# Kernel tuning notes

Hardware: AMD Instinct MI355X
Metric: run time of the kernel (lower is better)

The kernel has to match this reference:

```python
import jax, jax.numpy as jnp
import numpy as np

B, S, INP, HID = 64, 2048, 512, 512

def setup_inputs() -> dict:
    key = jax.random.key(0)
    ks = jax.random.split(key, 8)
    inp = jax.random.normal(ks[0], (B, INP), dtype=jnp.float32)
    context = jax.random.normal(ks[1], (B, S, INP), dtype=jnp.float32)
    mask = jax.random.randint(ks[2], (B, S), 0, 2) == 1  # True = masked out
    lim_l = 1.0 / np.sqrt(INP)
    Wl = jax.random.uniform(ks[3], (HID, INP), minval=-lim_l, maxval=lim_l, dtype=jnp.float32)
    bl = jax.random.uniform(ks[4], (HID,), minval=-lim_l, maxval=lim_l, dtype=jnp.float32)
    Wc = jax.random.uniform(ks[5], (HID, INP), minval=-lim_l, maxval=lim_l, dtype=jnp.float32)  # Conv1d k=1 weight squeezed
    bc = jax.random.uniform(ks[6], (HID,), minval=-lim_l, maxval=lim_l, dtype=jnp.float32)
    V = jax.random.uniform(ks[7], (HID,), minval=-1.0, maxval=1.0, dtype=jnp.float32)
    return {"inp": inp, "context": context, "mask": mask,
            "Wl": Wl, "bl": bl, "Wc": Wc, "bc": bc, "V": V}

def reference(inp, context, mask, Wl, bl, Wc, bc, V):
    # hid: [B, HID], broadcast over S
    hid = inp @ Wl.T + bl
    # 1x1 Conv1d over permuted context == per-position linear: [B, HID, S]
    ctx = jnp.einsum('bsi,hi->bhs', context, Wc) + bc[None, :, None]
    # additive attention scores: [B, S]
    att = jnp.einsum('h,bhs->bs', V, jnp.tanh(hid[:, :, None] + ctx))
    att = jnp.where(mask, -jnp.inf, att)
    alpha = jax.nn.softmax(att, axis=1)
    # context vector: [B, HID]
    hidden_state = jnp.einsum('bhs,bs->bh', ctx, alpha)
    return (hidden_state, alpha)
```

## Files before the change

kernel.cpp:

```cpp
#include <hip/hip_runtime.h>
#include <hip/hip_bf16.h>
#include <cstdint>
#include <cstddef>

#define B_   64
#define S_   2048
#define INP_ 512
#define HID_ 512

typedef float          floatx4  __attribute__((ext_vector_type(4)));
typedef __bf16         bf16x8   __attribute__((ext_vector_type(8)));
typedef unsigned short ushortx8 __attribute__((ext_vector_type(8)));

__device__ __forceinline__ unsigned short f2bf(float f) {
  unsigned u = __float_as_uint(f);
  u += 0x7FFFu + ((u >> 16) & 1u);
  return (unsigned short)(u >> 16);
}
__device__ __forceinline__ float fast_tanh(float x) {
  float u = __builtin_amdgcn_exp2f(x * 2.88539008177792681472f);
  return 1.0f - 2.0f * __builtin_amdgcn_rcpf(u + 1.0f);
}

__device__ __forceinline__ void gload_lds16(const float* g, float* l) {
  __builtin_amdgcn_global_load_lds(
      (const __attribute__((address_space(1))) unsigned int*)(const void*)g,
      (__attribute__((address_space(3))) unsigned int*)(void*)l, 16, 0, 0);
}

template<int NPART>
__global__ __launch_bounds__(256) void rowdot_kernel(
    const float* __restrict__ W, const float* __restrict__ bias,
    const float* __restrict__ vecs, float* __restrict__ out, int nch)
{
  __shared__ float vs[512];
  const int b = blockIdx.y, t = threadIdx.x;
  const int w = t >> 6, lane = t & 63;
  for (int i = t; i < 512; i += 256) {
    float s;
    if (NPART) {
      s = 0.0f;
      for (int c = 0; c < nch; ++c)
        s += vecs[((size_t)c * B_ + b) * INP_ + i];
    } else {
      s = vecs[(size_t)b * 512 + i];
    }
    vs[i] = s;
  }
  __syncthreads();
  float vl[8];
  #pragma unroll
  for (int j = 0; j < 8; ++j) vl[j] = vs[lane * 8 + j];
  const int h0 = blockIdx.x * 64 + w * 16;
  #pragma unroll
  for (int i = 0; i < 16; ++i) {
    const int h = h0 + i;
    const float4* wr = (const float4*)(W + (size_t)h * 512 + lane * 8);
    float4 w0 = wr[0], w1 = wr[1];
    float d = w0.x*vl[0] + w0.y*vl[1] + w0.z*vl[2] + w0.w*vl[3]
            + w1.x*vl[4] + w1.y*vl[5] + w1.z*vl[6] + w1.w*vl[7];
    #pragma unroll
    for (int off = 32; off; off >>= 1) d += __shfl_xor(d, off);
    if (lane == 0) out[(size_t)b * 512 + h] = bias[h] + d;
  }
}

__global__ void pack_wc_kernel(const float* __restrict__ Wc, unsigned short* __restrict__ pk)
{
  int g = blockIdx.x * 256 + threadIdx.x;
  int l = g & 63, ks = (g >> 6) & 15, m16 = g >> 10;
  int row = m16 * 16 + (l & 15);
  int kb  = ks * 32 + (l >> 4) * 8;
  const float4* s = (const float4*)(Wc + (size_t)row * 512 + kb);
  float4 a = s[0], c = s[1];
  ushortx8 o = { f2bf(a.x), f2bf(a.y), f2bf(a.z), f2bf(a.w),
                 f2bf(c.x), f2bf(c.y), f2bf(c.z), f2bf(c.w) };
  *(ushortx8*)(pk + (size_t)g * 8) = o;
}

__global__ __launch_bounds__(256, 2) void att_gemm_kernel(
    const float* __restrict__ context, const unsigned short* __restrict__ Wc_pk,
    const float* __restrict__ hid, const float* __restrict__ bc,
    const float* __restrict__ V, float* __restrict__ att)
{
  __shared__ alignas(16) float bsf[64 * 128];
  __shared__ float hid_sm[512];
  __shared__ float V_sm[512];
  __shared__ float bc_sm[512];
  __shared__ float att_sm[64];

  const int b    = blockIdx.y;
  const int s0   = blockIdx.x * 64;
  const int t    = threadIdx.x;
  const int lane = t & 63;
  const int w    = t >> 6;
  const int quad = lane >> 4;
  const int l15  = lane & 15;

  for (int i = t; i < 512; i += 256) {
    hid_sm[i] = hid[b * 512 + i];
    V_sm[i]   = V[i];
    bc_sm[i]  = bc[i];
  }
  if (t < 64) att_sm[t] = 0.0f;

  floatx4 acc[8][4];
  #pragma unroll
  for (int m = 0; m < 8; ++m)
    #pragma unroll
    for (int n = 0; n < 4; ++n) { floatx4 z = {0.f,0.f,0.f,0.f}; acc[m][n] = z; }

  const unsigned short* apBase = Wc_pk + (size_t)(w * 8) * 8192 + lane * 8;
  const float* src = context + ((size_t)b * S_ + s0) * INP_;

  for (int phase = 0; phase < 4; ++phase) {
    __syncthreads();
    #pragma unroll
    for (int i = 0; i < 8; ++i) {
      const int row = (w * 8 + i) * 2 + (lane >> 5);
      const int c   = (lane & 31) ^ (row & 7);
      gload_lds16(src + (size_t)row * INP_ + phase * 128 + c * 4,
                  &bsf[(w * 8 + i) * 256]);
    }
    __syncthreads();
    #pragma unroll
    for (int ksl = 0; ksl < 4; ++ksl) {
      const int ksg = phase * 4 + ksl;
      bf16x8 bfr[4];
      #pragma unroll
      for (int n = 0; n < 4; ++n) {
        const int row = n * 16 + l15;
        const int cb  = ksl * 8 + quad * 2;
        const int p0  = cb ^ (row & 7);
        const int p1  = (cb + 1) ^ (row & 7);
        floatx4 f0 = *(const floatx4*)(&bsf[row * 128 + p0 * 4]);
        floatx4 f1 = *(const floatx4*)(&bsf[row * 128 + p1 * 4]);
        bf16x8 r;
        r[0] = (__bf16)f0[0]; r[1] = (__bf16)f0[1];
        r[2] = (__bf16)f0[2]; r[3] = (__bf16)f0[3];
        r[4] = (__bf16)f1[0]; r[5] = (__bf16)f1[1];
        r[6] = (__bf16)f1[2]; r[7] = (__bf16)f1[3];
        bfr[n] = r;
      }
      #pragma unroll
      for (int m = 0; m < 8; ++m) {
        bf16x8 af = *(const bf16x8*)(apBase + (size_t)m * 8192 + (size_t)ksg * 512);
        #pragma unroll
        for (int n = 0; n < 4; ++n)
          acc[m][n] = __builtin_amdgcn_mfma_f32_16x16x32_bf16(af, bfr[n], acc[m][n], 0, 0, 0);
      }
    }
  }

  float attacc[4] = {0.f, 0.f, 0.f, 0.f};
  #pragma unroll
  for (int m = 0; m < 8; ++m) {
    const int hb = w * 128 + m * 16 + quad * 4;
    #pragma unroll
    for (int r = 0; r < 4; ++r) {
      const int h = hb + r;
      const float base = hid_sm[h] + bc_sm[h];
      const float vv = V_sm[h];
      #pragma unroll
      for (int n = 0; n < 4; ++n)
        attacc[n] += vv * fast_tanh(base + acc[m][n][r]);
    }
  }
  #pragma unroll
  for (int n = 0; n < 4; ++n) {
    float v = attacc[n];
    v += __shfl_xor(v, 16);
    v += __shfl_xor(v, 32);
    if (lane < 16) atomicAdd(&att_sm[n * 16 + l15], v);
  }
  __syncthreads();
  if (t < 64) att[b * S_ + s0 + t] = att_sm[t];
}

__global__ void softmax_kernel(const void* __restrict__ mask,
                               const float* __restrict__ att,
                               float* __restrict__ alpha)
{
  __shared__ int flags;
  __shared__ float red[8];
  const int b = blockIdx.x, t = threadIdx.x;
  const int lane = t & 63, w = t >> 6;
  if (t == 0) flags = 0;
  __syncthreads();
  int f = 0;
  const unsigned* mw = (const unsigned*)mask;
  for (int i = t; i < 512; i += 256) {
    unsigned v = mw[i];
    if (v > 1u) f |= 1;
    if (v != 0u && v != 0x3f800000u) f |= 2;
  }
  if (f) atomicOr(&flags, f);
  __syncthreads();
  const int fl = flags;
  const int mode = ((fl & 1) == 0) ? 0 : (((fl & 2) == 0) ? 1 : 2);

  float v[8]; bool msk[8];
  float vmax = -1e30f;
  #pragma unroll
  for (int i = 0; i < 8; ++i) {
    int idx = i * 256 + t;
    bool m;
    if (mode == 0)      m = ((const int*)mask)[b * S_ + idx] != 0;
    else if (mode == 1) m = ((const float*)mask)[b * S_ + idx] != 0.0f;
    else                m = ((const unsigned char*)mask)[b * S_ + idx] != 0;
    msk[i] = m;
    v[i] = att[b * S_ + idx];
    if (!m) vmax = fmaxf(vmax, v[i]);
  }
  #pragma unroll
  for (int off = 32; off; off >>= 1) vmax = fmaxf(vmax, __shfl_xor(vmax, off));
  if (lane == 0) red[w] = vmax;
  __syncthreads();
  vmax = fmaxf(fmaxf(red[0], red[1]), fmaxf(red[2], red[3]));

  float e[8], s = 0.0f;
  #pragma unroll
  for (int i = 0; i < 8; ++i) {
    e[i] = msk[i] ? 0.0f : __builtin_amdgcn_exp2f((v[i] - vmax) * 1.4426950408889634f);
    s += e[i];
  }
  #pragma unroll
  for (int off = 32; off; off >>= 1) s += __shfl_xor(s, off);
  if (lane == 0) red[4 + w] = s;
  __syncthreads();
  s = red[4] + red[5] + red[6] + red[7];
  float rinv = 1.0f / s;
  #pragma unroll
  for (int i = 0; i < 8; ++i)
    alpha[b * S_ + i * 256 + t] = e[i] * rinv;
}

__global__ __launch_bounds__(256) void cbar_kernel(
    const float* __restrict__ context, const float* __restrict__ alpha,
    float* __restrict__ partial, int rows)
{
  __shared__ float a_sm[2048];
  const int b = blockIdx.y, c = blockIdx.x, t = threadIdx.x;
  const int s0 = c * rows;
  for (int i = t; i < rows; i += 256) a_sm[i] = alpha[(size_t)b * S_ + s0 + i];
  __syncthreads();
  const float* base = context + ((size_t)b * S_ + s0) * INP_ + t * 2;
  float ax = 0.f, ay = 0.f;
  #pragma unroll 8
  for (int s = 0; s < rows; ++s) {
    float2 v = *(const float2*)(base + (size_t)s * INP_);
    float a = a_sm[s];
    ax = fmaf(a, v.x, ax);
    ay = fmaf(a, v.y, ay);
  }
  float2 o; o.x = ax; o.y = ay;
  *(float2*)(partial + ((size_t)c * B_ + b) * INP_ + t * 2) = o;
}

extern "C" void kernel_launch(void* const* d_in, const int* in_sizes, int n_in,
                              void* d_out, int out_size, void* d_ws, size_t ws_size,
                              hipStream_t stream)
{
  const float* inp     = (const float*)d_in[0];
  const float* context = (const float*)d_in[1];
  const void*  mask    = d_in[2];
  const float* Wl      = (const float*)d_in[3];
  const float* bl      = (const float*)d_in[4];
  const float* Wc      = (const float*)d_in[5];
  const float* bc      = (const float*)d_in[6];
  const float* V       = (const float*)d_in[7];

  float* hidden = (float*)d_out;
  float* alpha  = (float*)d_out + B_ * HID_;

  char* ws = (char*)d_ws;
  const size_t HIDW_BYTES = (size_t)B_ * HID_ * 4;
  const size_t ATT_BYTES  = (size_t)B_ * S_ * 4;
  const size_t PK_BYTES   = (size_t)HID_ * INP_ * 2;

  float* hid_ws      = (float*)ws;
  float* att_ws      = (float*)(ws + HIDW_BYTES);
  unsigned short* pk = (unsigned short*)(ws + HIDW_BYTES + ATT_BYTES);
  float* partial     = (float*)(ws + HIDW_BYTES + ATT_BYTES + PK_BYTES);

  const size_t rem = ws_size - (HIDW_BYTES + ATT_BYTES + PK_BYTES);
  int nch = 16;
  while (nch > 1 && (size_t)nch * B_ * INP_ * 4 > rem) nch >>= 1;
  const int rows = S_ / nch;

  rowdot_kernel<0><<<dim3(HID_ / 64, B_), 256, 0, stream>>>(Wl, bl, inp, hid_ws, 0);
  pack_wc_kernel<<<128, 256, 0, stream>>>(Wc, pk);
  att_gemm_kernel<<<dim3(S_ / 64, B_), 256, 0, stream>>>(context, pk, hid_ws, bc, V, att_ws);
  softmax_kernel<<<B_, 256, 0, stream>>>(mask, att_ws, alpha);
  cbar_kernel<<<dim3(nch, B_), 256, 0, stream>>>(context, alpha, partial, rows);
  rowdot_kernel<1><<<dim3(HID_ / 64, B_), 256, 0, stream>>>(Wc, bc, partial, hidden, nch);
}
```

Baseline: 551.2 us.

## Fuse prep and softmax kernels, drop LDS staging in attention GEMM, widen to 512 threads

Merges hid rowdot and Wc packing into one prep launch, and merges softmax into the context-weighted-sum kernel so each chunk block recomputes the softmax for its batch row. The attention GEMM now uses 512 threads with 4 M-tiles per wave and reads context straight from global memory instead of staging it through LDS. The number of S chunks also rises to 32. These cut launch count and LDS traffic, but every cbar block repeats the full softmax and the GEMM now does many uncoalesced global reads. The barrier inside the phase loop no longer guards anything.

```diff
diff --git a/kernel.cpp b/kernel.cpp
--- a/kernel.cpp
+++ b/kernel.cpp
@@ -22,23 +22,15 @@
   return 1.0f - 2.0f * __builtin_amdgcn_rcpf(u + 1.0f);
 }
 
-__device__ __forceinline__ void gload_lds16(const float* g, float* l) {
-  __builtin_amdgcn_global_load_lds(
-      (const __attribute__((address_space(1))) unsigned int*)(const void*)g,
-      (__attribute__((address_space(3))) unsigned int*)(void*)l, 16, 0, 0);
-}
-
-template<int NPART>
-__global__ __launch_bounds__(256) void rowdot_kernel(
+__device__ __forceinline__ void rowdot_body(
     const float* __restrict__ W, const float* __restrict__ bias,
-    const float* __restrict__ vecs, float* __restrict__ out, int nch)
-{
-  __shared__ float vs[512];
-  const int b = blockIdx.y, t = threadIdx.x;
+    const float* __restrict__ vecs, float* __restrict__ out,
+    int nch, int npart, int xo, int b, int t, float* vs)
+{
   const int w = t >> 6, lane = t & 63;
   for (int i = t; i < 512; i += 256) {
     float s;
-    if (NPART) {
+    if (npart) {
       s = 0.0f;
       for (int c = 0; c < nch; ++c)
         s += vecs[((size_t)c * B_ + b) * INP_ + i];
@@ -51,7 +43,7 @@
   float vl[8];
   #pragma unroll
   for (int j = 0; j < 8; ++j) vl[j] = vs[lane * 8 + j];
-  const int h0 = blockIdx.x * 64 + w * 16;
+  const int h0 = xo * 64 + w * 16;
   #pragma unroll
   for (int i = 0; i < 16; ++i) {
     const int h = h0 + i;
@@ -65,25 +57,42 @@
   }
 }
 
-__global__ void pack_wc_kernel(const float* __restrict__ Wc, unsigned short* __restrict__ pk)
-{
-  int g = blockIdx.x * 256 + threadIdx.x;
-  int l = g & 63, ks = (g >> 6) & 15, m16 = g >> 10;
-  int row = m16 * 16 + (l & 15);
-  int kb  = ks * 32 + (l >> 4) * 8;
-  const float4* s = (const float4*)(Wc + (size_t)row * 512 + kb);
-  float4 a = s[0], c = s[1];
-  ushortx8 o = { f2bf(a.x), f2bf(a.y), f2bf(a.z), f2bf(a.w),
-                 f2bf(c.x), f2bf(c.y), f2bf(c.z), f2bf(c.w) };
-  *(ushortx8*)(pk + (size_t)g * 8) = o;
-}
-
-__global__ __launch_bounds__(256, 2) void att_gemm_kernel(
+__global__ __launch_bounds__(256) void prep_kernel(
+    const float* __restrict__ inp, const float* __restrict__ Wl,
+    const float* __restrict__ bl, float* __restrict__ hid,
+    const float* __restrict__ Wc, unsigned short* __restrict__ pk)
+{
+  __shared__ float vs[512];
+  const int t = threadIdx.x;
+  if (blockIdx.x < 128) {
+    int g = blockIdx.x * 256 + t;
+    int l = g & 63, ks = (g >> 6) & 15, m16 = g >> 10;
+    int row = m16 * 16 + (l & 15);
+    int kb  = ks * 32 + (l >> 4) * 8;
+    const float4* s = (const float4*)(Wc + (size_t)row * 512 + kb);
+    float4 a = s[0], c = s[1];
+    ushortx8 o = { f2bf(a.x), f2bf(a.y), f2bf(a.z), f2bf(a.w),
+                   f2bf(c.x), f2bf(c.y), f2bf(c.z), f2bf(c.w) };
+    *(ushortx8*)(pk + (size_t)g * 8) = o;
+    return;
+  }
+  const int bx = blockIdx.x - 128;
+  rowdot_body(Wl, bl, inp, hid, 0, 0, bx & 7, bx >> 3, t, vs);
+}
+
+__global__ __launch_bounds__(256) void hiddendot_kernel(
+    const float* __restrict__ Wc, const float* __restrict__ bc,
+    const float* __restrict__ partial, float* __restrict__ hidden, int nch)
+{
+  __shared__ float vs[512];
+  rowdot_body(Wc, bc, partial, hidden, nch, 1, blockIdx.x, blockIdx.y, threadIdx.x, vs);
+}
+
+__global__ __launch_bounds__(512, 2) void att_gemm_kernel(
     const float* __restrict__ context, const unsigned short* __restrict__ Wc_pk,
     const float* __restrict__ hid, const float* __restrict__ bc,
     const float* __restrict__ V, float* __restrict__ att)
 {
-  __shared__ alignas(16) float bsf[64 * 128];
   __shared__ float hid_sm[512];
   __shared__ float V_sm[512];
   __shared__ float bc_sm[512];
@@ -97,44 +106,34 @@
   const int quad = lane >> 4;
   const int l15  = lane & 15;
 
-  for (int i = t; i < 512; i += 256) {
+  for (int i = t; i < 512; i += 512) {
     hid_sm[i] = hid[b * 512 + i];
     V_sm[i]   = V[i];
     bc_sm[i]  = bc[i];
   }
   if (t < 64) att_sm[t] = 0.0f;
 
-  floatx4 acc[8][4];
-  #pragma unroll
-  for (int m = 0; m < 8; ++m)
+  floatx4 acc[4][4];
+  #pragma unroll
+  for (int m = 0; m < 4; ++m)
     #pragma unroll
     for (int n = 0; n < 4; ++n) { floatx4 z = {0.f,0.f,0.f,0.f}; acc[m][n] = z; }
 
-  const unsigned short* apBase = Wc_pk + (size_t)(w * 8) * 8192 + lane * 8;
-  const float* src = context + ((size_t)b * S_ + s0) * INP_;
-
+  const unsigned short* apBase = Wc_pk + (size_t)(w * 4) * 8192 + (size_t)lane * 8;
+  const float* bp = context + ((size_t)b * S_ + s0) * INP_;
+
+  __syncthreads();
   for (int phase = 0; phase < 4; ++phase) {
-    __syncthreads();
-    #pragma unroll
-    for (int i = 0; i < 8; ++i) {
-      const int row = (w * 8 + i) * 2 + (lane >> 5);
-      const int c   = (lane & 31) ^ (row & 7);
-      gload_lds16(src + (size_t)row * INP_ + phase * 128 + c * 4,
-                  &bsf[(w * 8 + i) * 256]);
-    }
-    __syncthreads();
+    if (phase) __builtin_amdgcn_s_barrier();
     #pragma unroll
     for (int ksl = 0; ksl < 4; ++ksl) {
       const int ksg = phase * 4 + ksl;
       bf16x8 bfr[4];
       #pragma unroll
       for (int n = 0; n < 4; ++n) {
-        const int row = n * 16 + l15;
-        const int cb  = ksl * 8 + quad * 2;
-        const int p0  = cb ^ (row & 7);
-        const int p1  = (cb + 1) ^ (row & 7);
-        floatx4 f0 = *(const floatx4*)(&bsf[row * 128 + p0 * 4]);
-        floatx4 f1 = *(const floatx4*)(&bsf[row * 128 + p1 * 4]);
+        const float* p = bp + (size_t)(n * 16 + l15) * INP_ + phase * 128 + (ksl * 4 + quad) * 8;
+        floatx4 f0 = *(const floatx4*)p;
+        floatx4 f1 = *(const floatx4*)(p + 4);
         bf16x8 r;
         r[0] = (__bf16)f0[0]; r[1] = (__bf16)f0[1];
         r[2] = (__bf16)f0[2]; r[3] = (__bf16)f0[3];
@@ -143,7 +142,7 @@
         bfr[n] = r;
       }
       #pragma unroll
-      for (int m = 0; m < 8; ++m) {
+      for (int m = 0; m < 4; ++m) {
         bf16x8 af = *(const bf16x8*)(apBase + (size_t)m * 8192 + (size_t)ksg * 512);
         #pragma unroll
         for (int n = 0; n < 4; ++n)
@@ -154,8 +153,8 @@
 
   float attacc[4] = {0.f, 0.f, 0.f, 0.f};
   #pragma unroll
-  for (int m = 0; m < 8; ++m) {
-    const int hb = w * 128 + m * 16 + quad * 4;
+  for (int m = 0; m < 4; ++m) {
+    const int hb = w * 64 + m * 16 + quad * 4;
     #pragma unroll
     for (int r = 0; r < 4; ++r) {
       const int h = hb + r;
@@ -177,16 +176,21 @@
   if (t < 64) att[b * S_ + s0 + t] = att_sm[t];
 }
 
-__global__ void softmax_kernel(const void* __restrict__ mask,
-                               const float* __restrict__ att,
-                               float* __restrict__ alpha)
+__global__ __launch_bounds__(256) void cbar_sm_kernel(
+    const void* __restrict__ mask, const float* __restrict__ att,
+    const float* __restrict__ context, float* __restrict__ alpha,
+    float* __restrict__ partial, int rows)
 {
   __shared__ int flags;
   __shared__ float red[8];
-  const int b = blockIdx.x, t = threadIdx.x;
+  __shared__ float a_sm[256];
+  __shared__ float redbuf[1024];
+
+  const int b = blockIdx.y, c = blockIdx.x, t = threadIdx.x;
   const int lane = t & 63, w = t >> 6;
   if (t == 0) flags = 0;
   __syncthreads();
+
   int f = 0;
   const unsigned* mw = (const unsigned*)mask;
   for (int i = t; i < 512; i += 256) {
@@ -229,32 +233,41 @@
   if (lane == 0) red[4 + w] = s;
   __syncthreads();
   s = red[4] + red[5] + red[6] + red[7];
-  float rinv = 1.0f / s;
-  #pragma unroll
-  for (int i = 0; i < 8; ++i)
-    alpha[b * S_ + i * 256 + t] = e[i] * rinv;
-}
-
-__global__ __launch_bounds__(256) void cbar_kernel(
-    const float* __restrict__ context, const float* __restrict__ alpha,
-    float* __restrict__ partial, int rows)
-{
-  __shared__ float a_sm[2048];
-  const int b = blockIdx.y, c = blockIdx.x, t = threadIdx.x;
-  const int s0 = c * rows;
-  for (int i = t; i < rows; i += 256) a_sm[i] = alpha[(size_t)b * S_ + s0 + i];
-  __syncthreads();
-  const float* base = context + ((size_t)b * S_ + s0) * INP_ + t * 2;
-  float ax = 0.f, ay = 0.f;
+  const float rinv = 1.0f / s;
+
+  const int sbase = c * rows;
+  #pragma unroll
+  for (int i = 0; i < 8; ++i) {
+    int idx = i * 256 + t;
+    int off = idx - sbase;
+    if ((unsigned)off < (unsigned)rows) {
+      float a = e[i] * rinv;
+      alpha[(size_t)b * S_ + idx] = a;
+      a_sm[off] = a;
+    }
+  }
+  __syncthreads();
+
+  const int col = (t & 127) * 4, rp = t >> 7;
+  const float* base2 = context + ((size_t)b * S_ + sbase) * INP_ + col;
+  floatx4 a4 = {0.f, 0.f, 0.f, 0.f};
   #pragma unroll 8
-  for (int s = 0; s < rows; ++s) {
-    float2 v = *(const float2*)(base + (size_t)s * INP_);
-    float a = a_sm[s];
-    ax = fmaf(a, v.x, ax);
-    ay = fmaf(a, v.y, ay);
-  }
-  float2 o; o.x = ax; o.y = ay;
-  *(float2*)(partial + ((size_t)c * B_ + b) * INP_ + t * 2) = o;
+  for (int sidx = rp; sidx < rows; sidx += 2) {
+    floatx4 vv = *(const floatx4*)(base2 + (size_t)sidx * INP_);
+    float a = a_sm[sidx];
+    a4[0] = fmaf(a, vv[0], a4[0]);
+    a4[1] = fmaf(a, vv[1], a4[1]);
+    a4[2] = fmaf(a, vv[2], a4[2]);
+    a4[3] = fmaf(a, vv[3], a4[3]);
+  }
+  *(floatx4*)&redbuf[rp * 512 + col] = a4;
+  __syncthreads();
+  if (t < 128) {
+    floatx4 r0 = *(const floatx4*)&redbuf[t * 4];
+    floatx4 r1 = *(const floatx4*)&redbuf[512 + t * 4];
+    floatx4 o = r0 + r1;
+    *(floatx4*)&partial[((size_t)c * B_ + b) * INP_ + t * 4] = o;
+  }
 }
 
 extern "C" void kernel_launch(void* const* d_in, const int* in_sizes, int n_in,
@@ -284,14 +297,12 @@
   float* partial     = (float*)(ws + HIDW_BYTES + ATT_BYTES + PK_BYTES);
 
   const size_t rem = ws_size - (HIDW_BYTES + ATT_BYTES + PK_BYTES);
-  int nch = 16;
-  while (nch > 1 && (size_t)nch * B_ * INP_ * 4 > rem) nch >>= 1;
+  int nch = 32;
+  while (nch > 8 && (size_t)nch * B_ * INP_ * 4 > rem) nch >>= 1;
   const int rows = S_ / nch;
 
-  rowdot_kernel<0><<<dim3(HID_ / 64, B_), 256, 0, stream>>>(Wl, bl, inp, hid_ws, 0);
-  pack_wc_kernel<<<128, 256, 0, stream>>>(Wc, pk);
-  att_gemm_kernel<<<dim3(S_ / 64, B_), 256, 0, stream>>>(context, pk, hid_ws, bc, V, att_ws);
-  softmax_kernel<<<B_, 256, 0, stream>>>(mask, att_ws, alpha);
-  cbar_kernel<<<dim3(nch, B_), 256, 0, stream>>>(context, alpha, partial, rows);
-  rowdot_kernel<1><<<dim3(HID_ / 64, B_), 256, 0, stream>>>(Wc, bc, partial, hidden, nch);
-}
+  prep_kernel<<<640, 256, 0, stream>>>(inp, Wl, bl, hid_ws, Wc, pk);
+  att_gemm_kernel<<<dim3(S_ / 64, B_), 512, 0, stream>>>(context, pk, hid_ws, bc, V, att_ws);
+  cbar_sm_kernel<<<dim3(nch, B_), 256, 0, stream>>>(mask, att_ws, context, alpha, partial, rows);
+  hiddendot_kernel<<<dim3(HID_ / 64, B_), 256, 0, stream>>>(Wc, bc, partial, hidden, nch);
+}
```

Result: slower. 757.2 us (+37.4%).
